# Optimization experiments

Measured on AMD Instinct MI355X. Metric: run time of the kernel, lower is better.

The kernel has to match this reference:

```python
import jax, jax.numpy as jnp
import numpy as np

NUM_TOKENS = 4096
IN_FEATURES = 2560
OUT_FEATURES = 3328
GROUPS = 8
# fixed uneven per-expert token counts summing to NUM_TOKENS (tokens are
# pre-sorted by expert into contiguous segments, as grouped_gemm requires)
TOKENS_PER_EXPERT = np.array([700, 300, 900, 150, 512, 600, 420, 514], dtype=np.int64)
assert TOKENS_PER_EXPERT.sum() == NUM_TOKENS


def setup_inputs() -> dict:
    key = jax.random.key(0)
    k_x, k_w = jax.random.split(key)
    x = jax.random.normal(k_x, (NUM_TOKENS, IN_FEATURES), dtype=jnp.float32)
    # weight layout matches nn.Parameter(groups, in_features, out_features)
    w = jax.random.normal(k_w, (GROUPS, IN_FEATURES, OUT_FEATURES), dtype=jnp.float32)
    w = w * (1.0 / np.sqrt(IN_FEATURES))
    tokens_per_expert = jnp.asarray(TOKENS_PER_EXPERT)
    return {"input": x, "weight": w, "tokens_per_expert": tokens_per_expert}


def reference(input, weight, tokens_per_expert):
    # Grouped GEMM: out[s_g:e_g] = input[s_g:e_g] @ weight[g] for each expert g.
    # tokens_per_expert lives on host in the original grouped_gemm library
    # (batch_sizes must be a CPU tensor), so we treat it as host metadata.
    sizes = np.asarray(tokens_per_expert)
    offsets = np.concatenate([[0], np.cumsum(sizes)])
    groups = weight.shape[0]
    outs = [input[offsets[g]:offsets[g + 1]] @ weight[g] for g in range(groups)]
    return jnp.concatenate(outs, axis=0)  # [num_tokens, out_features]
```

## Files before the change

kernel.cpp:

```cpp
#include <hip/hip_runtime.h>
#include <hip/hip_bf16.h>


#define KDIM 2560
#define NDIM 3328
#define BM 128
#define BN 128
#define BK 32
#define KITERS (KDIM / BK)
#define MAX_SLOTS 122
#define GRID_X (8 * MAX_SLOTS)

typedef __attribute__((ext_vector_type(8))) short bf16x8;
typedef __attribute__((ext_vector_type(4))) float f32x4;

__constant__ int c_tiles[8]  = {6,3,8,2,4,5,4,5};
__constant__ int c_mtbase[8] = {0,6,9,17,19,23,28,32};
__constant__ int c_row0[37] = {
    0,128,256,384,512,640,
    700,828,956,
    1000,1128,1256,1384,1512,1640,1768,1896,
    1900,2028,
    2050,2178,2306,2434,
    2562,2690,2818,2946,3074,
    3162,3290,3418,3546,
    3582,3710,3838,3966,4094};
__constant__ int c_nrows[37] = {
    128,128,128,128,128,60,
    128,128,44,
    128,128,128,128,128,128,128,4,
    128,22,
    128,128,128,128,
    128,128,128,128,88,
    128,128,128,36,
    128,128,128,128,2};

__constant__ int r_nruns[8]    = {1,2,1,3,1,3,1,3};
__constant__ int r_g[8][3]     = {{2,0,0},{2,3,0},{0,0,0},{0,1,3},{5,0,0},{5,4,3},{7,0,0},{7,6,3}};
__constant__ int r_nt0[8][3]   = {{0,0,0},{15,0,0},{0,0,0},{20,0,16},{0,0,0},{24,0,19},{0,0,0},{24,0,22}};
__constant__ int r_ncols[8][3] = {{15,0,0},{11,16,0},{20,0,0},{6,26,3},{24,0,0},{2,26,3},{24,0,0},{2,26,4}};

__device__ __forceinline__ unsigned pk2(float a, float b) {
    __hip_bfloat162 h = __float22bfloat162_rn(make_float2(a, b));
    unsigned r;
    __builtin_memcpy(&r, &h, sizeof(r));
    return r;
}

__global__ __launch_bounds__(256, 2) void ggemm_kernel(
    const float* __restrict__ X, const float* __restrict__ W,
    float* __restrict__ Out)
{
    const int b = blockIdx.x;
    const int x = b & 7;
    const int s = b >> 3;

    int g = -1, nt = 0, m = 0;
    {
        int base = 0;
        const int nr = r_nruns[x];
#pragma unroll
        for (int r = 0; r < 3; ++r) {
            if (r < nr && g < 0) {
                const int g_  = r_g[x][r];
                const int tg  = c_tiles[g_];
                const int len = r_ncols[x][r] * tg;
                if (s < base + len) {
                    const int off = s - base;
                    const int c   = off / tg;
                    m  = off - c * tg;
                    nt = r_nt0[x][r] + c;
                    g  = g_;
                }
                base += len;
            }
        }
    }
    if (g < 0) return;

    const int mt    = c_mtbase[g] + m;
    const int row0  = c_row0[mt];
    const int nrows = c_nrows[mt];
    const int n0    = nt * BN;

    __shared__ __align__(16) __hip_bfloat16 As[BM * BK];
    __shared__ __align__(16) __hip_bfloat16 Bs[BN * BK];

    const int tid = threadIdx.x;
    const int t8  = tid >> 3;
    const int t7  = tid & 7;

    const float* xbase = X + (size_t)(row0 + t8) * KDIM + t7 * 4;
    bool aval[4];
#pragma unroll
    for (int ss = 0; ss < 4; ++ss) aval[ss] = (t8 + 32 * ss) < nrows;
    const int a_lds0 = t8 * BK + (((t7 >> 1) ^ (t8 & 3)) * 8) + (t7 & 1) * 4;

    const float* wbase = W + (size_t)g * (KDIM * NDIM) + (t7 * 4) * NDIM + n0 + t8 * 4;

    float4 Areg[4];
    float4 Breg[4];

    auto load_tiles = [&](int kt) {
        const int ko = kt * BK;
#pragma unroll
        for (int ss = 0; ss < 4; ++ss) {
            float4 v = make_float4(0.f, 0.f, 0.f, 0.f);
            if (aval[ss]) v = *(const float4*)(xbase + (size_t)(ss * 32) * KDIM + ko);
            Areg[ss] = v;
        }
#pragma unroll
        for (int i = 0; i < 4; ++i)
            Breg[i] = *(const float4*)(wbase + (size_t)(ko + i) * NDIM);
    };

    const int lane = tid & 63;
    const int wv   = tid >> 6;
    const int wm   = wv & 1;
    const int wn   = wv >> 1;
    const int lm   = lane & 15;
    const int quad = lane >> 4;
    const int kg   = quad ^ (lm & 3);

    f32x4 acc[4][4];
#pragma unroll
    for (int i = 0; i < 4; ++i)
#pragma unroll
        for (int j = 0; j < 4; ++j)
            acc[i][j] = (f32x4){0.f, 0.f, 0.f, 0.f};

    load_tiles(0);

    for (int kt = 0; kt < KITERS; ++kt) {
        __syncthreads();

#pragma unroll
        for (int ss = 0; ss < 4; ++ss) {
            uint2 u;
            u.x = pk2(Areg[ss].x, Areg[ss].y);
            u.y = pk2(Areg[ss].z, Areg[ss].w);
            *(uint2*)&As[a_lds0 + ss * 32 * BK] = u;
        }
        {
            const float* b0 = reinterpret_cast<const float*>(&Breg[0]);
            const float* b1 = reinterpret_cast<const float*>(&Breg[1]);
            const float* b2 = reinterpret_cast<const float*>(&Breg[2]);
            const float* b3 = reinterpret_cast<const float*>(&Breg[3]);
#pragma unroll
            for (int j = 0; j < 4; ++j) {
                uint2 u;
                u.x = pk2(b0[j], b1[j]);
                u.y = pk2(b2[j], b3[j]);
                const int idx = (t8 * 4 + j) * BK + (((t7 >> 1) ^ j) * 8) + (t7 & 1) * 4;
                *(uint2*)&Bs[idx] = u;
            }
        }
        __syncthreads();

        if (kt + 1 < KITERS) load_tiles(kt + 1);

        bf16x8 af[4], bfr[4];
#pragma unroll
        for (int mi = 0; mi < 4; ++mi)
            af[mi] = *(const bf16x8*)&As[(wm * 64 + mi * 16 + lm) * BK + kg * 8];
#pragma unroll
        for (int ni = 0; ni < 4; ++ni)
            bfr[ni] = *(const bf16x8*)&Bs[(wn * 64 + ni * 16 + lm) * BK + kg * 8];
#pragma unroll
        for (int mi = 0; mi < 4; ++mi)
#pragma unroll
            for (int ni = 0; ni < 4; ++ni)
                acc[mi][ni] = __builtin_amdgcn_mfma_f32_16x16x32_bf16(
                    af[mi], bfr[ni], acc[mi][ni], 0, 0, 0);
    }

#pragma unroll
    for (int mi = 0; mi < 4; ++mi) {
#pragma unroll
        for (int r = 0; r < 4; ++r) {
            const int ml = wm * 64 + mi * 16 + quad * 4 + r;
            if (ml < nrows) {
                float* orow = Out + (size_t)(row0 + ml) * NDIM + n0 + wn * 64 + lm;
#pragma unroll
                for (int ni = 0; ni < 4; ++ni)
                    orow[ni * 16] = acc[mi][ni][r];
            }
        }
    }
}

extern "C" void kernel_launch(void* const* d_in, const int* in_sizes, int n_in,
                              void* d_out, int out_size, void* d_ws, size_t ws_size,
                              hipStream_t stream) {
    const float* X = (const float*)d_in[0];
    const float* W = (const float*)d_in[1];
    float* O = (float*)d_out;
    ggemm_kernel<<<dim3(GRID_X, 1, 1), 256, 0, stream>>>(X, W, O);
}
```

Baseline: 570.5 us.

## Double-buffer LDS tiles and prefetch two K-steps ahead in registers

Splits the shared-memory A/B tiles into two buffers and keeps two register sets of fp32 tiles, so global loads run two K-steps ahead. Staging the next tile into one LDS buffer overlaps with MFMA compute on the other, which removes one barrier per K-step. The cost is twice the LDS and extra registers for the second prefetch set. Under launch_bounds(256,2) that could cause spills or lower occupancy.

Measured after the change: 648.6 us. 13.7% more time.

```diff
diff --git a/kernel.cpp b/kernel.cpp
--- a/kernel.cpp
+++ b/kernel.cpp
@@ -83,8 +83,8 @@
     const int nrows = c_nrows[mt];
     const int n0    = nt * BN;
 
-    __shared__ __align__(16) __hip_bfloat16 As[BM * BK];
-    __shared__ __align__(16) __hip_bfloat16 Bs[BN * BK];
+    __shared__ __align__(16) __hip_bfloat16 As[2][BM * BK];
+    __shared__ __align__(16) __hip_bfloat16 Bs[2][BN * BK];
 
     const int tid = threadIdx.x;
     const int t8  = tid >> 3;
@@ -97,22 +97,6 @@
     const int a_lds0 = t8 * BK + (((t7 >> 1) ^ (t8 & 3)) * 8) + (t7 & 1) * 4;
 
     const float* wbase = W + (size_t)g * (KDIM * NDIM) + (t7 * 4) * NDIM + n0 + t8 * 4;
-
-    float4 Areg[4];
-    float4 Breg[4];
-
-    auto load_tiles = [&](int kt) {
-        const int ko = kt * BK;
-#pragma unroll
-        for (int ss = 0; ss < 4; ++ss) {
-            float4 v = make_float4(0.f, 0.f, 0.f, 0.f);
-            if (aval[ss]) v = *(const float4*)(xbase + (size_t)(ss * 32) * KDIM + ko);
-            Areg[ss] = v;
-        }
-#pragma unroll
-        for (int i = 0; i < 4; ++i)
-            Breg[i] = *(const float4*)(wbase + (size_t)(ko + i) * NDIM);
-    };
 
     const int lane = tid & 63;
     const int wv   = tid >> 6;
@@ -122,6 +106,61 @@
     const int quad = lane >> 4;
     const int kg   = quad ^ (lm & 3);
 
+    float4 Ar0[4], Br0[4], Ar1[4], Br1[4];
+
+#define LOAD_TILES(kt, AR, BR) do {                                            \
+    const int ko_ = (kt) * BK;                                                 \
+    _Pragma("unroll")                                                          \
+    for (int ss = 0; ss < 4; ++ss) {                                           \
+        float4 v_ = make_float4(0.f, 0.f, 0.f, 0.f);                           \
+        if (aval[ss]) v_ = *(const float4*)(xbase + (size_t)(ss * 32) * KDIM + ko_); \
+        AR[ss] = v_;                                                           \
+    }                                                                          \
+    _Pragma("unroll")                                                          \
+    for (int i_ = 0; i_ < 4; ++i_)                                             \
+        BR[i_] = *(const float4*)(wbase + (size_t)(ko_ + i_) * NDIM);          \
+} while (0)
+
+#define STAGE(AR, BR, ASb, BSb) do {                                           \
+    _Pragma("unroll")                                                          \
+    for (int ss = 0; ss < 4; ++ss) {                                           \
+        uint2 u_;                                                              \
+        u_.x = pk2(AR[ss].x, AR[ss].y);                                        \
+        u_.y = pk2(AR[ss].z, AR[ss].w);                                        \
+        *(uint2*)&(ASb)[a_lds0 + ss * 32 * BK] = u_;                           \
+    }                                                                          \
+    {                                                                          \
+        const float* b0_ = reinterpret_cast<const float*>(&BR[0]);             \
+        const float* b1_ = reinterpret_cast<const float*>(&BR[1]);             \
+        const float* b2_ = reinterpret_cast<const float*>(&BR[2]);             \
+        const float* b3_ = reinterpret_cast<const float*>(&BR[3]);             \
+        _Pragma("unroll")                                                      \
+        for (int j_ = 0; j_ < 4; ++j_) {                                       \
+            uint2 u_;                                                          \
+            u_.x = pk2(b0_[j_], b1_[j_]);                                      \
+            u_.y = pk2(b2_[j_], b3_[j_]);                                      \
+            const int idx_ = (t8 * 4 + j_) * BK + (((t7 >> 1) ^ j_) * 8) + (t7 & 1) * 4; \
+            *(uint2*)&(BSb)[idx_] = u_;                                        \
+        }                                                                      \
+    }                                                                          \
+} while (0)
+
+#define COMPUTE(ASb, BSb) do {                                                 \
+    bf16x8 af_[4], bf_[4];                                                     \
+    _Pragma("unroll")                                                          \
+    for (int mi = 0; mi < 4; ++mi)                                             \
+        af_[mi] = *(const bf16x8*)&(ASb)[(wm * 64 + mi * 16 + lm) * BK + kg * 8]; \
+    _Pragma("unroll")                                                          \
+    for (int ni = 0; ni < 4; ++ni)                                             \
+        bf_[ni] = *(const bf16x8*)&(BSb)[(wn * 64 + ni * 16 + lm) * BK + kg * 8]; \
+    _Pragma("unroll")                                                          \
+    for (int mi = 0; mi < 4; ++mi)                                             \
+        _Pragma("unroll")                                                      \
+        for (int ni = 0; ni < 4; ++ni)                                         \
+            acc[mi][ni] = __builtin_amdgcn_mfma_f32_16x16x32_bf16(             \
+                af_[mi], bf_[ni], acc[mi][ni], 0, 0, 0);                       \
+} while (0)
+
     f32x4 acc[4][4];
 #pragma unroll
     for (int i = 0; i < 4; ++i)
@@ -129,49 +168,21 @@
         for (int j = 0; j < 4; ++j)
             acc[i][j] = (f32x4){0.f, 0.f, 0.f, 0.f};
 
-    load_tiles(0);
-
-    for (int kt = 0; kt < KITERS; ++kt) {
+    LOAD_TILES(0, Ar0, Br0);
+    LOAD_TILES(1, Ar1, Br1);
+    STAGE(Ar0, Br0, As[0], Bs[0]);
+    __syncthreads();
+
+    for (int kt = 0; kt < KITERS; kt += 2) {
+        if (kt + 2 < KITERS) LOAD_TILES(kt + 2, Ar0, Br0);
+        STAGE(Ar1, Br1, As[1], Bs[1]);
+        COMPUTE(As[0], Bs[0]);
         __syncthreads();
 
-#pragma unroll
-        for (int ss = 0; ss < 4; ++ss) {
-            uint2 u;
-            u.x = pk2(Areg[ss].x, Areg[ss].y);
-            u.y = pk2(Areg[ss].z, Areg[ss].w);
-            *(uint2*)&As[a_lds0 + ss * 32 * BK] = u;
-        }
-        {
-            const float* b0 = reinterpret_cast<const float*>(&Breg[0]);
-            const float* b1 = reinterpret_cast<const float*>(&Breg[1]);
-            const float* b2 = reinterpret_cast<const float*>(&Breg[2]);
-            const float* b3 = reinterpret_cast<const float*>(&Breg[3]);
-#pragma unroll
-            for (int j = 0; j < 4; ++j) {
-                uint2 u;
-                u.x = pk2(b0[j], b1[j]);
-                u.y = pk2(b2[j], b3[j]);
-                const int idx = (t8 * 4 + j) * BK + (((t7 >> 1) ^ j) * 8) + (t7 & 1) * 4;
-                *(uint2*)&Bs[idx] = u;
-            }
-        }
+        if (kt + 3 < KITERS) LOAD_TILES(kt + 3, Ar1, Br1);
+        if (kt + 2 < KITERS) STAGE(Ar0, Br0, As[0], Bs[0]);
+        COMPUTE(As[1], Bs[1]);
         __syncthreads();
-
-        if (kt + 1 < KITERS) load_tiles(kt + 1);
-
-        bf16x8 af[4], bfr[4];
-#pragma unroll
-        for (int mi = 0; mi < 4; ++mi)
-            af[mi] = *(const bf16x8*)&As[(wm * 64 + mi * 16 + lm) * BK + kg * 8];
-#pragma unroll
-        for (int ni = 0; ni < 4; ++ni)
-            bfr[ni] = *(const bf16x8*)&Bs[(wn * 64 + ni * 16 + lm) * BK + kg * 8];
-#pragma unroll
-        for (int mi = 0; mi < 4; ++mi)
-#pragma unroll
-            for (int ni = 0; ni < 4; ++ni)
-                acc[mi][ni] = __builtin_amdgcn_mfma_f32_16x16x32_bf16(
-                    af[mi], bfr[ni], acc[mi][ni], 0, 0, 0);
     }
 
 #pragma unroll
@@ -187,6 +198,9 @@
             }
         }
     }
+#undef LOAD_TILES
+#undef STAGE
+#undef COMPUTE
 }
 
 extern "C" void kernel_launch(void* const* d_in, const int* in_sizes, int n_in,
```
